# Kernel optimization log

Hardware: AMD Instinct MI355X
Metric: run time of the kernel (lower is better)

The kernel has to match this reference:

```python
import jax, jax.numpy as jnp
import numpy as np

N, E, M, NC, G = 20000, 640000, 200000, 50000, 512
VOCAB, IN, HID, OUT, NCLS = 8, 64, 128, 128, 2
EPS = 1e-5
SLOPE = 0.01


def _bn(x, g, b):
    # BatchNorm1d in training mode: biased batch statistics (matches torch normalization)
    m = jnp.mean(x, axis=0)
    v = jnp.var(x, axis=0)
    return g * (x - m) * jax.lax.rsqrt(v + EPS) + b


def _seg_softmax(a, ids, ns):
    m = jax.ops.segment_max(a, ids, num_segments=ns)
    ex = jnp.exp(a - m[ids])
    s = jax.ops.segment_sum(ex, ids, num_segments=ns)
    return ex / s[ids]


def _seg_mean(x, ids, ns):
    s = jax.ops.segment_sum(x, ids, num_segments=ns)
    c = jax.ops.segment_sum(jnp.ones((x.shape[0], 1), x.dtype), ids, num_segments=ns)
    return s / jnp.maximum(c, 1.0)


def setup_inputs() -> dict:
    key = jax.random.key(0)
    ks = jax.random.split(key, 24)

    def nrm(k, shape, fan_in):
        return jax.random.normal(k, shape, jnp.float32) * np.float32(1.0 / np.sqrt(fan_in))

    inp = {
        "sub_x": jax.random.randint(ks[0], (N, 1), 0, VOCAB),
        "sub_edge_index": jax.random.randint(ks[1], (2, E), 0, N),
        "batch": jnp.sort(jax.random.randint(ks[2], (N,), 0, G)),
        "cycle_seg_id": jnp.sort(jax.random.randint(ks[3], (M,), 0, NC)),
        "cycle_edge_idx": jax.random.randint(ks[4], (M,), 0, E),
        # embedding + mlp_feature (nn.Linear with bias)
        "emb": nrm(ks[5], (VOCAB, IN), 1),
        "w1": nrm(ks[6], (2 * IN, 2 * IN), 2 * IN), "b1": jnp.zeros((2 * IN,), jnp.float32),
        "w2": nrm(ks[7], (2 * IN, HID), 2 * IN), "b2": jnp.zeros((HID,), jnp.float32),
        "g0": jnp.ones((HID,), jnp.float32), "beta0": jnp.zeros((HID,), jnp.float32),
        # bond_agg_layer (bias-free linears)
        "watt_b": nrm(ks[8], (HID,), HID),
        "wb1": nrm(ks[9], (HID, OUT), HID), "wb2": nrm(ks[10], (OUT, OUT), OUT),
        "g1": jnp.ones((OUT,), jnp.float32), "beta1": jnp.zeros((OUT,), jnp.float32),
        # cycle_agg_layer
        "watt_c": nrm(ks[11], (HID,), HID),
        "wc1": nrm(ks[12], (HID, OUT), HID), "wc2": nrm(ks[13], (OUT, OUT), OUT),
        "g2": jnp.ones((OUT,), jnp.float32), "beta2": jnp.zeros((OUT,), jnp.float32),
        # edge_agg_layer
        "we1": nrm(ks[14], (HID, OUT), HID), "we2": nrm(ks[15], (OUT, OUT), OUT),
        "wl1": nrm(ks[16], (OUT, OUT), OUT), "wl2": nrm(ks[17], (OUT, OUT), OUT),
        "g3": jnp.ones((OUT,), jnp.float32), "beta3": jnp.zeros((OUT,), jnp.float32),
        # graph_agg_layer
        "wg1": nrm(ks[18], (OUT, OUT), OUT), "wg2": nrm(ks[19], (OUT, OUT), OUT),
        "g4": jnp.ones((OUT,), jnp.float32), "beta4": jnp.zeros((OUT,), jnp.float32),
        "wout": nrm(ks[20], (OUT, NCLS), OUT),
    }
    return inp


def reference(sub_x, sub_edge_index, batch, cycle_seg_id, cycle_edge_idx,
              emb, w1, b1, w2, b2, g0, beta0,
              watt_b, wb1, wb2, g1, beta1,
              watt_c, wc1, wc2, g2, beta2,
              we1, we2, wl1, wl2, g3, beta3,
              wg1, wg2, g4, beta4, wout):
    src, dst = sub_edge_index[0], sub_edge_index[1]
    x0 = emb[sub_x[:, 0]]                                    # [N, IN]
    h = jnp.concatenate([x0[src], x0[dst]], axis=-1)         # [E, 2*IN]
    h = (h @ w1 + b1) @ w2 + b2                              # [E, HID]
    h = jax.nn.gelu(_bn(h, g0, beta0), approximate=False)
    # bond aggregation: per-target-node segment softmax attention + scatter-mean
    ab = jax.nn.leaky_relu(h @ watt_b, SLOPE)                # [E]
    ab = _seg_softmax(ab, dst, N)
    bond = _seg_mean(ab[:, None] * h, dst, N)                # [N, HID]
    bond = jax.nn.gelu(_bn((bond @ wb1) @ wb2, g1, beta1), approximate=False)
    # cycle aggregation over membership list (cycle_seg_id: cycle id, cycle_edge_idx: edge idx)
    hc = h[cycle_edge_idx]                                   # [M, HID]
    ac = jax.nn.leaky_relu(hc @ watt_c, SLOPE)               # [M]
    ac = _seg_softmax(ac, cycle_seg_id, NC)
    cyc = _seg_mean(ac[:, None] * hc, cycle_seg_id, NC)      # [NC, HID]
    cyc = jax.nn.gelu(_bn((cyc @ wc1) @ wc2, g2, beta2), approximate=False)
    # edge update
    e = (h @ we1) @ we2                                      # [E, OUT]
    xc = jax.ops.segment_sum(cyc[cycle_seg_id], cycle_edge_idx, num_segments=E)
    e = ((e + bond[src] + bond[dst] + xc) @ wl1) @ wl2
    e = jax.nn.gelu(_bn(e, g3, beta3), approximate=False)
    # graph readout: sum edges by graph of their source node
    gsum = jax.ops.segment_sum(e, batch[src], num_segments=G)  # [G, OUT]
    gsum = (gsum @ wg1) @ wg2
    gsum = jax.nn.gelu(_bn(gsum, g4, beta4), approximate=False)
    return gsum @ wout                                       # [G, NCLS]
```

## Files before the change

kernel.cpp:

```cpp
#include <hip/hip_runtime.h>
#include <hip/hip_bf16.h>

typedef __hip_bfloat16 bf16;

__device__ __forceinline__ float b2f(bf16 v){ return __bfloat162float(v); }
__device__ __forceinline__ bf16  f2b(float v){ return __float2bfloat16(v); }
__device__ __forceinline__ float erf_fast(float x){
  const float ax=fabsf(x);
  const float t=__builtin_amdgcn_rcpf(1.f+0.3275911f*ax);
  const float p=t*(0.254829592f+t*(-0.284496736f+t*(1.421413741f+t*(-1.453152027f+t*1.061405429f))));
  const float r=1.f-p*__expf(-ax*ax);
  return copysignf(r,x);
}
__device__ __forceinline__ float geluf(float x){ return 0.5f*x*(1.0f+erf_fast(x*0.70710678118654752f)); }
__device__ __forceinline__ float lreluf(float x){ return x>0.f? x : 0.01f*x; }
__device__ __forceinline__ float bflo(unsigned u){ return __builtin_bit_cast(float,(unsigned)((u&0xFFFFu)<<16)); }
__device__ __forceinline__ float bfhi(unsigned u){ return __builtin_bit_cast(float,(unsigned)(u&0xFFFF0000u)); }
__device__ __forceinline__ unsigned packbf(float a, float b){
  bf16 ha=f2b(a), hb=f2b(b);
  return (unsigned)__builtin_bit_cast(unsigned short,ha) | ((unsigned)__builtin_bit_cast(unsigned short,hb)<<16);
}

__device__ __forceinline__ int detect_bf16(const unsigned int* words){
  int hits=0;
  for(int i=0;i<64;i++){
    unsigned u=words[i], lo=u&0xFFFFu, e=(lo>>7)&0xFFu;
    if(lo==0u || (e>=100u && e<=140u)) hits++;
  }
  return (hits>=40)?1:0;
}

struct ConvertArgs { const void* src[28]; float* dst[28]; int n[28]; };
__global__ __launch_bounds__(256) void k_convert(ConvertArgs A, const unsigned int* embw,
                                                 int* flag, float* zp, int zn){
  const int id=blockIdx.x;
  if(id<28){
    const int bf=detect_bf16(embw);
    if(id==0 && threadIdx.x==0) *flag=bf;
    const void* s=A.src[id];
    float* d=A.dst[id];
    const int n=A.n[id];
    if(bf){
      const bf16* sp=(const bf16*)s;
      for(int i=threadIdx.x;i<n;i+=256) d[i]=b2f(sp[i]);
    } else {
      const float* sp=(const float*)s;
      for(int i=threadIdx.x;i<n;i+=256) d[i]=sp[i];
    }
  } else {
    const int zb=id-28;
    int i=zb*256+threadIdx.x;
    const int stride=1024*256;
    for(;i<zn;i+=stride) zp[i]=0.f;
  }
}

struct GemmTasks5 { const float* X[5]; const float* W[5]; float* Y[5]; };

template<int K>
__global__ __launch_bounds__(256) void k_rowgemm(GemmTasks5 T5, int rows, int mode, int xPacked,
    const float* stS, const float* stQ, float invRows,
    const float* gam, const float* bet,
    float* outS, float* outQ, unsigned* Yp, const float* partsIn)
{
  constexpr int KH = K/2;
  const int task = blockIdx.y;
  const float* Xv = T5.X[task];
  const float* W  = T5.W[task];
  float* Y = T5.Y[task];
  const int tid = threadIdx.x, c = tid & 127, kh = tid >> 7;
  __shared__ float redSQ[256];
  if(mode==1 && partsIn){
    float s=0.f;
    for(int k=0;k<64;k++) s+=partsIn[k*256+tid];
    redSQ[tid]=s;
    __syncthreads();
  }
  float wreg[KH];
  #pragma unroll
  for(int i=0;i<KH;i++) wreg[i]=W[(kh*KH+i)*128+c];
  __shared__ float xls[8*K];
  __shared__ float part[2*8*128];
  float ls=0.f, lq=0.f;
  const int nbatch=(rows+7)>>3;
  for (int b=blockIdx.x; b<nbatch; b+=gridDim.x){
    const int base=b*8;
    for (int idx=tid; idx<8*K; idx+=256){
      const int row=idx/K, k=idx-row*K, r=base+row;
      float v=0.f;
      if (r<rows){
        if(xPacked){
          const unsigned u=((const unsigned*)Xv)[(size_t)r*(K/2)+(k>>1)];
          v = (k&1) ? bfhi(u) : bflo(u);
        } else {
          v = Xv[(size_t)r*K+k];
        }
        if (mode==1){
          const float sv = partsIn ? redSQ[k]     : stS[k];
          const float qv = partsIn ? redSQ[128+k] : stQ[k];
          float mn=sv*invRows;
          float vr=fmaxf(qv*invRows-mn*mn,0.f);
          float sc=gam[k]*rsqrtf(vr+1e-5f);
          float sh=bet[k]-mn*sc;
          v=geluf(v*sc+sh);
        }
      }
      xls[idx]=v;
    }
    __syncthreads();
    #pragma unroll
    for (int rr=0;rr<8;rr++){
      const float* xp=&xls[rr*K+kh*KH];
      float acc=0.f;
      #pragma unroll
      for (int j=0;j<KH;j+=4){
        const float4 xv=*(const float4*)(xp+j);
        acc += wreg[j]*xv.x + wreg[j+1]*xv.y + wreg[j+2]*xv.z + wreg[j+3]*xv.w;
      }
      part[kh*1024 + rr*128 + c]=acc;
    }
    __syncthreads();
    if (Yp==nullptr){
      #pragma unroll
      for (int q=0;q<4;q++){
        const int r=kh*4+q, row=base+r;
        if (row<rows){
          float y=part[r*128+c]+part[1024+r*128+c];
          Y[row*128+c]=y;
          ls+=y; lq+=y*y;
        }
      }
      __syncthreads();
    } else {
      if constexpr (K==128){
        #pragma unroll
        for (int q=0;q<4;q++){
          const int r=kh*4+q, row=base+r;
          float y=0.f;
          if (row<rows){
            y=part[r*128+c]+part[1024+r*128+c];
            ls+=y; lq+=y*y;
          }
          xls[r*128+c]=y;
        }
        __syncthreads();
        for (int idx=tid; idx<512; idx+=256){
          const int r2=idx>>6, j=idx&63, row=base+r2;
          if(row<rows) Yp[(size_t)row*64+j]=packbf(xls[r2*128+2*j],xls[r2*128+2*j+1]);
        }
        __syncthreads();
      }
    }
  }
  if (outS){ atomicAdd(&outS[c],ls); atomicAdd(&outQ[c],lq); }
}

struct RGDual {
  const float* x0; int rows0; int pk0; float inv0; const float* g0; const float* b0;
  unsigned* yp0; const float* parts0;
  const float* x1; int rows1; int pk1; float inv1; const float* g1; const float* b1;
  unsigned* yp1; const float* parts1;
  const float* W;
};
__global__ __launch_bounds__(512) void k_rowgemm_dual(RGDual D)
{
  const int tid = threadIdx.x, c = tid & 127, kq = tid >> 7;
  __shared__ float scs0[128], shs0[128], scs1[128], shs1[128];
  if(tid<256){
    const int t=tid>>7, k=tid&127;
    const float* partsIn = t ? D.parts1 : D.parts0;
    float s=0.f,q=0.f;
    for(int j=0;j<64;j++){ s+=partsIn[j*256+k]; }
    for(int j=0;j<64;j++){ q+=partsIn[j*256+128+k]; }
    const float invRows = t ? D.inv1 : D.inv0;
    const float gam = (t ? D.g1 : D.g0)[k];
    const float bet = (t ? D.b1 : D.b0)[k];
    const float mn=s*invRows;
    const float vr=fmaxf(q*invRows-mn*mn,0.f);
    const float sc=gam*rsqrtf(vr+1e-5f);
    const float sh=bet-mn*sc;
    if(t){ scs1[k]=sc; shs1[k]=sh; } else { scs0[k]=sc; shs0[k]=sh; }
  }
  __syncthreads();
  float wreg[32];
  #pragma unroll
  for(int i=0;i<32;i++) wreg[i]=D.W[(kq*32+i)*128+c];
  __shared__ float xls[8*128];
  __shared__ float part[4*8*128];
  const int TB0=(D.rows0+7)>>3, TB1=(D.rows1+7)>>3;
  const int TBT=TB0+TB1;
  for (int gb=blockIdx.x; gb<TBT; gb+=gridDim.x){
    const int t1=(gb>=TB0);
    const int b = t1 ? gb-TB0 : gb;
    const float* Xv = t1 ? D.x1 : D.x0;
    const int rows  = t1 ? D.rows1 : D.rows0;
    const int xPacked = t1 ? D.pk1 : D.pk0;
    unsigned* Yp = t1 ? D.yp1 : D.yp0;
    const float* scs = t1 ? scs1 : scs0;
    const float* shs = t1 ? shs1 : shs0;
    const int base=b*8;
    for (int idx=tid; idx<8*128; idx+=512){
      const int row=idx>>7, k=idx&127, r=base+row;
      float v=0.f;
      if (r<rows){
        if(xPacked){
          const unsigned u=((const unsigned*)Xv)[(size_t)r*64+(k>>1)];
          v = (k&1) ? bfhi(u) : bflo(u);
        } else {
          v = Xv[(size_t)r*128+k];
        }
        v=geluf(v*scs[k]+shs[k]);
      }
      xls[idx]=v;
    }
    __syncthreads();
    float acc[8];
    #pragma unroll
    for (int rr=0;rr<8;rr++){
      const float* xp=&xls[rr*128+kq*32];
      float a=0.f;
      #pragma unroll
      for (int j=0;j<32;j+=4){
        const float4 xv=*(const float4*)(xp+j);
        a += wreg[j]*xv.x + wreg[j+1]*xv.y + wreg[j+2]*xv.z + wreg[j+3]*xv.w;
      }
      acc[rr]=a;
    }
    #pragma unroll
    for (int rr=0;rr<8;rr++) part[kq*1024+rr*128+c]=acc[rr];
    __syncthreads();
    #pragma unroll
    for (int q=0;q<2;q++){
      const int r=kq*2+q, row=base+r;
      const float y=(part[r*128+c]+part[1024+r*128+c])
                   +(part[2048+r*128+c]+part[3072+r*128+c]);
      const float y2=__shfl_xor(y,1,64);
      if(((tid&1)==0) && row<rows) Yp[(size_t)row*64+(c>>1)]=packbf(y,y2);
    }
  }
}

__global__ __launch_bounds__(256) void k_table_T(const float* emb, const float* w1, const float* b1,
                                                 const float* w2, const float* b2, float* T)
{
  __shared__ float A[2048];
  const int tid=threadIdx.x;
  for (int idx=tid; idx<2048; idx+=256){
    const int half=idx>>10, rem=idx&1023, s=rem>>7, j=rem&127;
    float acc=0.f;
    for(int k=0;k<64;k++) acc += emb[s*64+k]*w1[(half*64+k)*128+j];
    A[idx]=acc;
  }
  __syncthreads();
  const int o=tid&127;
  for(int rr=tid>>7; rr<8; rr+=2){
    const int r=blockIdx.x*8+rr, s=r>>3, d=r&7;
    float acc=b2[o];
    for(int j=0;j<128;j++){
      float t1=A[s*128+j]+A[1024+d*128+j]+b1[j];
      acc+=t1*w2[j*128+o];
    }
    T[r*128+o]=acc;
  }
}

#define SCH 1024

__global__ __launch_bounds__(256) void k_edge_code(const int* sx, const int* src, const int* dst,
    const int* batch, unsigned char* code, unsigned short* gg, int* cnt64, int* ns,
    int* blockHist, int E)
{
  __shared__ int hist[64];
  __shared__ int gh[512];
  const int tid=threadIdx.x;
  if(tid<64) hist[tid]=0;
  for(int i=tid;i<512;i+=256) gh[i]=0;
  __syncthreads();
  const int base=blockIdx.x*SCH;
  #pragma unroll
  for(int u=0;u<SCH/256;u++){
    const int e=base+u*256+tid;
    if(e<E){
      const int s_=src[e], d_=dst[e];
      const int sc=sx[s_], dc=sx[d_];
      const int cd=sc*8+dc;
      code[e]=(unsigned char)cd;
      const int gb=batch[s_];
      gg[e]=(unsigned short)gb;
      atomicAdd(&hist[cd],1);
      atomicAdd(&ns[d_*8+sc],1);
      atomicAdd(&gh[gb],1);
    }
  }
  __syncthreads();
  if(tid<64){ int h=hist[tid]; if(h) atomicAdd(&cnt64[tid],h); }
  for(int i=tid;i<512;i+=256) blockHist[blockIdx.x*512+i]=gh[i];
}

__global__ __launch_bounds__(256) void k_gscan_col(int* blockHist, int* gtot, int NB){
  const int g=blockIdx.x;
  const int tid=threadIdx.x;
  __shared__ int sd[256];
  int run=0;
  for(int base=0;base<NB;base+=256){
    const int b=base+tid;
    const int v=(b<NB)?blockHist[(size_t)b*512+g]:0;
    sd[tid]=v; __syncthreads();
    for(int d=1;d<256;d<<=1){ int t=(tid>=d)?sd[tid-d]:0; __syncthreads(); sd[tid]+=t; __syncthreads(); }
    const int incl=sd[tid];
    const int tot=sd[255];
    if(b<NB) blockHist[(size_t)b*512+g]=run+incl-v;
    __syncthreads();
    run+=tot;
  }
  if(tid==0) gtot[g]=run;
}

__global__ __launch_bounds__(256) void k_gscatter(const unsigned short* gg, const int* blockHist,
    const int* gtot, const unsigned char* code, const int* src, const int* dst,
    unsigned short* sortedG, int* posE, unsigned long long* recP, int E){
  __shared__ int baseg[512];
  __shared__ int sg[512];
  const int tid=threadIdx.x;
  for(int i=tid;i<512;i+=256) sg[i]=gtot[i];
  __syncthreads();
  for(int d=1;d<512;d<<=1){
    int t0[2];
    for(int i=tid,j=0;i<512;i+=256,j++) t0[j]=(i>=d)?sg[i-d]:0;
    __syncthreads();
    for(int i=tid,j=0;i<512;i+=256,j++) sg[i]+=t0[j];
    __syncthreads();
  }
  for(int i=tid;i<512;i+=256) baseg[i]=blockHist[blockIdx.x*512+i]+sg[i]-gtot[i];
  __syncthreads();
  const int base=blockIdx.x*SCH;
  for(int i=tid;i<SCH;i+=256){
    const int e=base+i;
    if(e<E){
      const int g=gg[e];
      const int p=atomicAdd(&baseg[g],1);
      sortedG[p]=(unsigned short)g;
      posE[e]=p;
      recP[p]=(unsigned long long)code[e] | ((unsigned long long)(unsigned)src[e]<<8)
            | ((unsigned long long)(unsigned)dst[e]<<32);
    }
  }
}

__global__ __launch_bounds__(256) void k_htable(const float* T, const int* cnt64,
    const float* g0, const float* beta0, const float* wattb, const float* wattc,
    float* h_table, float* abt, float* act, float* ea, int E)
{
  __shared__ float h[64*132];
  __shared__ float cw[64];
  const int tid=threadIdx.x;
  if(tid<64) cw[tid]=(float)cnt64[tid];
  __syncthreads();
  const int c=tid&127;
  const float invE=1.f/(float)E;
  float s=0.f,q=0.f;
  for(int r2=0;r2<64;r2++){ float v=T[r2*128+c]; float w=cw[r2]; s+=w*v; q+=w*v*v; }
  const float mn=s*invE, vr=fmaxf(q*invE-mn*mn,0.f);
  const float sc=g0[c]*rsqrtf(vr+1e-5f), sh=beta0[c]-mn*sc;
  for(int r=tid>>7; r<64; r+=2){
    float v=geluf(T[r*128+c]*sc+sh);
    h[r*132+c]=v;
    h_table[r*128+c]=v;
  }
  __syncthreads();
  if(tid<64){
    float sb=0.f,scc=0.f;
    for(int k=0;k<128;k++){ float hv=h[tid*132+k]; sb+=hv*wattb[k]; scc+=hv*wattc[k]; }
    const float ab_=lreluf(sb), ac_=lreluf(scc);
    abt[tid]=ab_; act[tid]=ac_;
    float mx=ac_;
    #pragma unroll
    for(int o=1;o<64;o<<=1) mx=fmaxf(mx,__shfl_xor(mx,o,64));
    ea[tid]=expf(ac_-mx);
  }
}

__global__ __launch_bounds__(256) void k_cycle_hist(const int* cseg, const int* cidx,
    const unsigned char* code, const int* posE, int* nsc, int* cntP, int M)
{
  const int base=blockIdx.x*1024+threadIdx.x;
  #pragma unroll
  for(int u=0;u<4;u++){
    const int m=base+u*256;
    if(m<M){
      const int e=cidx[m];
      atomicAdd(&nsc[cseg[m]*64 + (int)code[e]],1);
      atomicAdd(&cntP[posE[e]],1);
    }
  }
}

__global__ __launch_bounds__(256) void k_bond(const int* ns, const int* sx, const float* abt,
    const float* hWb, float* bm, float* parts, int N)
{
  const int tid=threadIdx.x, c=tid&127, grp=tid>>7;
  float ls=0.f,lq=0.f;
  const int base=blockIdx.x*16+grp*8;
  for(int i=0;i<8;i++){
    const int n=base+i;
    if(n>=N) break;
    const int d=sx[n];
    float cnt=0.f, mx=-1e30f, nsv[8];
    #pragma unroll
    for(int s=0;s<8;s++){ float v=(float)ns[n*8+s]; nsv[s]=v; cnt+=v; if(v>0.f) mx=fmaxf(mx,abt[s*8+d]); }
    float y=0.f;
    if(cnt>0.f){
      float ssum=0.f, ex[8];
      #pragma unroll
      for(int s=0;s<8;s++){ ex[s]= nsv[s]>0.f ? nsv[s]*expf(abt[s*8+d]-mx) : 0.f; ssum+=ex[s]; }
      const float inv=1.f/(ssum*cnt);
      #pragma unroll
      for(int s=0;s<8;s++){ if(ex[s]>0.f) y += (ex[s]*inv)*hWb[(s*8+d)*128+c]; }
    }
    bm[n*128+c]=y;
    ls+=y; lq+=y*y;
  }
  __shared__ float sS[128], sQ[128];
  if(tid<128){ sS[tid]=0.f; sQ[tid]=0.f; }
  __syncthreads();
  atomicAdd(&sS[c],ls); atomicAdd(&sQ[c],lq);
  __syncthreads();
  if(tid<128){
    float* slot=&parts[(size_t)(blockIdx.x&63)*256];
    atomicAdd(&slot[tid],sS[tid]); atomicAdd(&slot[128+tid],sQ[tid]);
  }
}

__global__ __launch_bounds__(256) void k_cyc(const int* nsc, const float* ea,
    const float* hWc, unsigned* ucm, float* parts, int NC)
{
  const int tid=threadIdx.x, c=tid&127, kh=tid>>7;
  const int lane=tid&63;
  const int wv4=tid>>6;
  const float eaL=ea[lane];
  float wreg[32];
  #pragma unroll
  for(int i=0;i<32;i++) wreg[i]=hWc[(kh*32+i)*128+c]*ea[kh*32+i];
  __shared__ float cnts[512];
  __shared__ float part[2*8*128];
  __shared__ float invcs[8];
  float ls=0.f,lq=0.f;
  const int nbatch=(NC+7)>>3;
  for(int b=blockIdx.x;b<nbatch;b+=gridDim.x){
    const int base=b*8;
    for(int i=tid;i<512;i+=256){
      const int seg=base+(i>>6);
      cnts[i] = (seg<NC) ? (float)nsc[(size_t)seg*64+(i&63)] : 0.f;
    }
    __syncthreads();
    #pragma unroll
    for(int rr2=0;rr2<2;rr2++){
      const int r=wv4*2+rr2;
      const float n=cnts[r*64+lane];
      float S=n*eaL, C=n;
      #pragma unroll
      for(int o=1;o<64;o<<=1){ S+=__shfl_xor(S,o,64); C+=__shfl_xor(C,o,64); }
      if(lane==0) invcs[r]=(C>0.f&&S>0.f)?1.f/(S*C):0.f;
    }
    #pragma unroll
    for(int rr=0;rr<8;rr++){
      const float* xp=&cnts[rr*64+kh*32];
      float acc=0.f;
      #pragma unroll
      for(int j=0;j<32;j+=4){
        const float4 xv=*(const float4*)(xp+j);
        acc += wreg[j]*xv.x + wreg[j+1]*xv.y + wreg[j+2]*xv.z + wreg[j+3]*xv.w;
      }
      part[kh*1024+rr*128+c]=acc;
    }
    __syncthreads();
    #pragma unroll
    for(int q=0;q<4;q++){
      const int r=kh*4+q, row=base+r;
      float y=0.f;
      if(row<NC){
        y=(part[r*128+c]+part[1024+r*128+c])*invcs[r];
        ls+=y; lq+=y*y;
      }
      const float y2=__shfl_xor(y,1,64);
      if(((lane&1)==0) && row<NC) ucm[(size_t)row*64+(c>>1)]=packbf(y,y2);
    }
    __syncthreads();
  }
  __shared__ float sS[128], sQ[128];
  if(tid<128){ sS[tid]=0.f; sQ[tid]=0.f; }
  __syncthreads();
  atomicAdd(&sS[c],ls); atomicAdd(&sQ[c],lq);
  __syncthreads();
  if(tid<128){
    float* slot=&parts[(size_t)(blockIdx.x&63)*256];
    atomicAdd(&slot[tid],sS[tid]); atomicAdd(&slot[128+tid],sQ[tid]);
  }
}

__global__ __launch_bounds__(256) void k_scan_block(const int* cntP, int* blkSum, int E){
  __shared__ int sd[256];
  const int tid=threadIdx.x, base=blockIdx.x*1024;
  int s=0;
  for(int q=0;q<4;q++){ int i=base+tid*4+q; if(i<E) s+=cntP[i]; }
  sd[tid]=s; __syncthreads();
  for(int d=1;d<256;d<<=1){ int t=(tid>=d)?sd[tid-d]:0; __syncthreads(); sd[tid]+=t; __syncthreads(); }
  if(tid==255) blkSum[blockIdx.x]=sd[255];
}

__global__ __launch_bounds__(256) void k_scan_mid(const int* blkSum, int* blkOff, int nb){
  __shared__ int sd[1024];
  const int tid=threadIdx.x;
  for(int i=tid;i<1024;i+=256) sd[i]=(i<nb)?blkSum[i]:0;
  __syncthreads();
  for(int d=1;d<1024;d<<=1){
    int t[4];
    for(int i=tid,j=0;i<1024;i+=256,j++) t[j]=(i>=d)?sd[i-d]:0;
    __syncthreads();
    for(int i=tid,j=0;i<1024;i+=256,j++) sd[i]+=t[j];
    __syncthreads();
  }
  for(int i=tid;i<nb;i+=256) blkOff[i]=sd[i]-blkSum[i];
}

__global__ __launch_bounds__(256) void k_scan_write(const int* cntP, const int* blkOff,
                                                    int* offP, int E, int M){
  __shared__ int sd[256];
  const int tid=threadIdx.x, base=blockIdx.x*1024;
  int v[4]; int s=0;
  for(int q=0;q<4;q++){ int i=base+tid*4+q; v[q]=(i<E)?cntP[i]:0; s+=v[q]; }
  sd[tid]=s; __syncthreads();
  for(int d=1;d<256;d<<=1){ int t=(tid>=d)?sd[tid-d]:0; __syncthreads(); sd[tid]+=t; __syncthreads(); }
  int run=blkOff[blockIdx.x]+sd[tid]-s;
  for(int q=0;q<4;q++){ int i=base+tid*4+q; if(i<E) offP[i]=run; run+=v[q]; }
  if(blockIdx.x==0&&tid==0) offP[E]=M;
}

__global__ __launch_bounds__(256) void k_place(const int* cseg, const int* cidx, const int* posE,
                                               const int* offP, int* cursor, int* entrySeg, int M){
  const int base=blockIdx.x*1024+threadIdx.x;
  #pragma unroll
  for(int u=0;u<4;u++){
    const int m=base+u*256;
    if(m<M){
      const int p=posE[cidx[m]];
      const int pos=offP[p]+atomicAdd(&cursor[p],1);
      entrySeg[pos]=cseg[m];
    }
  }
}

__global__ __launch_bounds__(256) void k_pass1_store(const unsigned long long* recP,
    const float* eLt, const unsigned* ubond, const unsigned* ucyc,
    const int* offP, const int* entrySeg, unsigned* vbuf, float* parts,
    int E, int upx)
{
  const int tid=threadIdx.x;
  const int lane=tid&63, wave=tid>>6;
  const int xcd=blockIdx.x&7;
  const int wix=(blockIdx.x>>3)*4+wave;
  const int NU=(E+15)>>4;
  int u0=xcd*upx + (int)(((long long)wix*(long long)upx)>>10);
  int u1=xcd*upx + (int)(((long long)(wix+1)*(long long)upx)>>10);
  if(u0>NU)u0=NU; if(u1>NU)u1=NU;
  int e=u0*16; const int e1=(u1*16<E)?u1*16:E;
  float lsx=0.f,lsy=0.f,lqx=0.f,lqy=0.f;
  while(e<e1){
    int nv=e1-e; if(nv>64)nv=64;
    const int t=e+((lane<nv)?lane:(nv-1));
    const unsigned long long r0=recP[t];
    const unsigned rlo=(unsigned)r0, rhi=(unsigned)(r0>>32);
    const int oa0=offP[t], ob0=offP[t+1];
    int i=0;
    for(; i+8<=nv; i+=8){
      unsigned lo[8],hi[8]; int a[8],b[8];
      #pragma unroll
      for(int q=0;q<8;q++){
        lo[q]=(unsigned)__builtin_amdgcn_readlane((int)rlo,i+q);
        hi[q]=(unsigned)__builtin_amdgcn_readlane((int)rhi,i+q);
        a[q]=__builtin_amdgcn_readlane(oa0,i+q);
        b[q]=__builtin_amdgcn_readlane(ob0,i+q);
      }
      float2 ea[8]; unsigned ub[8],ud[8];
      #pragma unroll
      for(int q=0;q<8;q++){
        ea[q]=((const float2*)(eLt+(size_t)(lo[q]&0xFFu)*128))[lane];
        ub[q]=ubond[(size_t)(lo[q]>>8)*64+lane];
        ud[q]=ubond[(size_t)hi[q]*64+lane];
      }
      #pragma unroll
      for(int q=0;q<8;q++){
        float x=ea[q].x+bflo(ub[q])+bflo(ud[q]);
        float y=ea[q].y+bfhi(ub[q])+bfhi(ud[q]);
        for(int j=a[q];j<b[q];j++){
          const unsigned w=ucyc[(size_t)entrySeg[j]*64+lane];
          x+=bflo(w); y+=bfhi(w);
        }
        lsx+=x; lqx+=x*x; lsy+=y; lqy+=y*y;
        vbuf[(size_t)(e+i+q)*64+lane]=packbf(x,y);
      }
    }
    for(; i<nv; i++){
      const unsigned lo=(unsigned)__builtin_amdgcn_readlane((int)rlo,i);
      const unsigned hi=(unsigned)__builtin_amdgcn_readlane((int)rhi,i);
      const int a=__builtin_amdgcn_readlane(oa0,i);
      const int b=__builtin_amdgcn_readlane(ob0,i);
      const float2 ea2=((const float2*)(eLt+(size_t)(lo&0xFFu)*128))[lane];
      const unsigned ub=ubond[(size_t)(lo>>8)*64+lane];
      const unsigned ud=ubond[(size_t)hi*64+lane];
      float x=ea2.x+bflo(ub)+bflo(ud);
      float y=ea2.y+bfhi(ub)+bfhi(ud);
      for(int j=a;j<b;j++){
        const unsigned w=ucyc[(size_t)entrySeg[j]*64+lane];
        x+=bflo(w); y+=bfhi(w);
      }
      lsx+=x; lqx+=x*x; lsy+=y; lqy+=y*y;
      vbuf[(size_t)(e+i)*64+lane]=packbf(x,y);
    }
    e+=nv;
  }
  __shared__ float sS[128], sQ[128];
  if(tid<128){ sS[tid]=0.f; sQ[tid]=0.f; }
  __syncthreads();
  const int c0=lane*2;
  atomicAdd(&sS[c0],lsx); atomicAdd(&sS[c0+1],lsy);
  atomicAdd(&sQ[c0],lqx); atomicAdd(&sQ[c0+1],lqy);
  __syncthreads();
  if(tid<128){
    float* slot=&parts[(size_t)(blockIdx.x&63)*256];
    atomicAdd(&slot[tid],sS[tid]); atomicAdd(&slot[128+tid],sQ[tid]);
  }
}

__global__ __launch_bounds__(256) void k_pass2_stream(const uint2* vbuf2,
    const unsigned short* sortedG, const float* parts,
    const float* g3, const float* beta3, float* gsum, int E)
{
  __shared__ float sSQ[256];
  const int tid=threadIdx.x;
  {
    float s=0.f;
    #pragma unroll 8
    for(int k=0;k<64;k++) s+=parts[k*256+tid];
    sSQ[tid]=s;
  }
  __syncthreads();
  const int lane=tid&63, wave=tid>>6;
  const int half=lane>>5;
  const int l32=lane&31;
  const int cb=l32*4;
  const float invE=1.f/(float)E;
  float sc[4],sh[4];
  #pragma unroll
  for(int k2=0;k2<4;k2++){
    const int c=cb+k2;
    float mn=sSQ[c]*invE, vr=fmaxf(sSQ[128+c]*invE-mn*mn,0.f);
    sc[k2]=g3[c]*rsqrtf(vr+1e-5f); sh[k2]=beta3[c]-mn*sc[k2];
  }
  const int wix=blockIdx.x*4+wave;
  const int NP=(E+1)>>1;
  int i0=(int)(((long long)wix*(long long)NP)>>13)*2;
  int i1=(int)(((long long)(wix+1)*(long long)NP)>>13)*2;
  if(i1>E)i1=E;
  int gcur=-1; float a0=0.f,a1=0.f,a2=0.f,a3=0.f;
  int i=i0;
  for(; i+32<=i1; i+=32){
    int gq[16]; uint2 uq[16];
    #pragma unroll
    for(int q=0;q<16;q++) gq[q]=sortedG[i+2*q+half];
    #pragma unroll
    for(int q=0;q<16;q++) uq[q]=vbuf2[(size_t)(i+2*q+half)*32+l32];
    #pragma unroll
    for(int q=0;q<16;q++){
      if(gq[q]!=gcur){
        if(gcur>=0){
          atomicAdd(&gsum[gcur*128+cb+0],a0); atomicAdd(&gsum[gcur*128+cb+1],a1);
          atomicAdd(&gsum[gcur*128+cb+2],a2); atomicAdd(&gsum[gcur*128+cb+3],a3);
        }
        gcur=gq[q]; a0=a1=a2=a3=0.f;
      }
      a0+=geluf(fmaf(bflo(uq[q].x),sc[0],sh[0]));
      a1+=geluf(fmaf(bfhi(uq[q].x),sc[1],sh[1]));
      a2+=geluf(fmaf(bflo(uq[q].y),sc[2],sh[2]));
      a3+=geluf(fmaf(bfhi(uq[q].y),sc[3],sh[3]));
    }
  }
  for(; i<i1; i+=2){
    const int p=i+half;
    if(p>=E) break;
    const int g=sortedG[p];
    const uint2 u=vbuf2[(size_t)p*32+l32];
    if(g!=gcur){
      if(gcur>=0){
        atomicAdd(&gsum[gcur*128+cb+0],a0); atomicAdd(&gsum[gcur*128+cb+1],a1);
        atomicAdd(&gsum[gcur*128+cb+2],a2); atomicAdd(&gsum[gcur*128+cb+3],a3);
      }
      gcur=g; a0=a1=a2=a3=0.f;
    }
    a0+=geluf(fmaf(bflo(u.x),sc[0],sh[0])); a1+=geluf(fmaf(bfhi(u.x),sc[1],sh[1]));
    a2+=geluf(fmaf(bflo(u.y),sc[2],sh[2])); a3+=geluf(fmaf(bfhi(u.y),sc[3],sh[3]));
  }
  if(gcur>=0){
    atomicAdd(&gsum[gcur*128+cb+0],a0); atomicAdd(&gsum[gcur*128+cb+1],a1);
    atomicAdd(&gsum[gcur*128+cb+2],a2); atomicAdd(&gsum[gcur*128+cb+3],a3);
  }
}

__global__ __launch_bounds__(256) void k_out(const float* gw, const float* st4S, const float* st4Q,
    const float* g4, const float* beta4, const float* wout, void* out, const int* flag, int G)
{
  const int lane=threadIdx.x&63;
  const int r=blockIdx.x*4 + (threadIdx.x>>6);
  const float invG=1.f/(float)G;
  float a0=0.f,a1=0.f;
  #pragma unroll
  for(int h=0;h<2;h++){
    const int k=lane+64*h;
    const float mn=st4S[k]*invG;
    const float vr=fmaxf(st4Q[k]*invG-mn*mn,0.f);
    const float sc=g4[k]*rsqrtf(vr+1e-5f), sh=beta4[k]-mn*sc;
    const float v=geluf(gw[r*128+k]*sc+sh);
    a0+=v*wout[k*2+0]; a1+=v*wout[k*2+1];
  }
  for(int o=1;o<64;o<<=1){ a0+=__shfl_xor(a0,o,64); a1+=__shfl_xor(a1,o,64); }
  if(lane==0){
    if(*flag){ ((bf16*)out)[r*2+0]=f2b(a0); ((bf16*)out)[r*2+1]=f2b(a1); }
    else     { ((float*)out)[r*2+0]=a0;     ((float*)out)[r*2+1]=a1; }
  }
}

extern "C" void kernel_launch(void* const* d_in, const int* in_sizes, int n_in,
                              void* d_out, int out_size, void* d_ws, size_t ws_size,
                              hipStream_t stream)
{
  const int N  = in_sizes[0];
  const int E  = in_sizes[1]/2;
  const int M  = in_sizes[3];
  const int NC = 50000;
  const int G  = 512;

  const int* sub_x=(const int*)d_in[0];
  const int* src=(const int*)d_in[1];
  const int* dst=src+E;
  const int* batch=(const int*)d_in[2];
  const int* cseg=(const int*)d_in[3];
  const int* cidx=(const int*)d_in[4];

  char* ws=(char*)d_ws;
  size_t off=0;
  auto carve=[&](size_t bytes)->char*{ char* p=ws+off; off=(off+bytes+255)&~(size_t)255; return p; };

  size_t ftot=0;
  for(int i=0;i<28;i++) ftot += (size_t)in_sizes[5+i];
  float* stage=(float*)carve(ftot*4);
  float* fin[28];
  { size_t so=0; for(int i=0;i<28;i++){ fin[i]=stage+so; so+=(size_t)in_sizes[5+i]; } }
  const float *emb_f=fin[0], *w1_f=fin[1], *b1_f=fin[2], *w2_f=fin[3], *b2_f=fin[4],
              *g0_f=fin[5], *beta0_f=fin[6], *wattb_f=fin[7], *wb1_f=fin[8], *wb2_f=fin[9],
              *g1_f=fin[10], *beta1_f=fin[11], *wattc_f=fin[12], *wc1_f=fin[13], *wc2_f=fin[14],
              *g2_f=fin[15], *beta2_f=fin[16], *we1_f=fin[17], *we2_f=fin[18], *wl1_f=fin[19],
              *wl2_f=fin[20], *g3_f=fin[21], *beta3_f=fin[22], *wg1_f=fin[23], *wg2_f=fin[24],
              *g4_f=fin[25], *beta4_f=fin[26], *wout_f=fin[27];

  int* flag=(int*)carve(256);
  float* Wb =(float*)carve(65536);
  float* Wc =(float*)carve(65536);
  float* Wl =(float*)carve(65536);
  float* Wg =(float*)carve(65536);
  float* We =(float*)carve(65536);
  float* Wel=(float*)carve(65536);
  float* T      =(float*)carve(64*128*4);
  float* h_table=(float*)carve(64*128*4);
  float* hWb    =(float*)carve(64*128*4);
  float* hWc    =(float*)carve(64*128*4);
  float* eLt    =(float*)carve(64*128*4);
  float* abt=(float*)carve(256);
  float* act=(float*)carve(256);
  float* eaT=(float*)carve(256);
  float* bm   =(float*)carve((size_t)N*128*4);
  unsigned* ucm=(unsigned*)carve((size_t)NC*64*4);
  unsigned* ubond=(unsigned*)carve((size_t)N*64*4);
  unsigned* ucyc =(unsigned*)carve((size_t)NC*64*4);
  unsigned char* code=(unsigned char*)carve((size_t)E);
  unsigned short* gg=(unsigned short*)carve((size_t)E*2);
  unsigned short* sortedG=(unsigned short*)carve((size_t)E*2);
  int*   posE  =(int*)carve((size_t)E*4);
  unsigned long long* recP=(unsigned long long*)carve((size_t)E*8);
  int*   offP  =(int*)carve((size_t)(E+1)*4);
  int*   entrySeg=(int*)carve((size_t)M*4);
  int*   blkSum=(int*)carve(4096);
  int*   blkOff=(int*)carve(4096);
  int*   gtot  =(int*)carve(2048);
  const int NB=(E+SCH-1)/SCH;
  int*   blockHist=(int*)carve((size_t)NB*512*4);
  float* gw  =(float*)carve((size_t)G*128*4);

  const size_t zStart=off;
  int*   cnt64=(int*)carve(256);
  float* stats=(float*)carve(4096);
  float* st4S=stats+6*128, *st4Q=stats+7*128;
  float* parts1=(float*)carve(64*256*4);
  float* parts2=(float*)carve(64*256*4);
  float* parts3=(float*)carve(64*256*4);
  float* gsum=(float*)carve((size_t)G*128*4);
  int*   ns   =(int*)carve((size_t)N*8*4);
  int*   nsc  =(int*)carve((size_t)NC*64*4);
  int*   cntP =(int*)carve((size_t)E*4);
  int*   cursor=(int*)carve((size_t)E*4);
  const size_t zEnd=off;

  unsigned* vbuf=(unsigned*)carve((size_t)E*64*4);
  const int haveV = (off <= ws_size) ? 1 : 0;
  (void)n_in; (void)out_size;

  {
    ConvertArgs A{};
    for(int i=0;i<28;i++){ A.src[i]=d_in[5+i]; A.dst[i]=fin[i]; A.n[i]=in_sizes[5+i]; }
    k_convert<<<28+1024,256,0,stream>>>(A,(const unsigned int*)d_in[5],flag,
                                        (float*)(ws+zStart),(int)((zEnd-zStart)/4));
  }

  k_table_T<<<8,256,0,stream>>>(emb_f,w1_f,b1_f,w2_f,b2_f,T);

  {
    GemmTasks5 t{};
    t.X[0]=wb1_f; t.W[0]=wb2_f; t.Y[0]=Wb;
    t.X[1]=wc1_f; t.W[1]=wc2_f; t.Y[1]=Wc;
    t.X[2]=wl1_f; t.W[2]=wl2_f; t.Y[2]=Wl;
    t.X[3]=wg1_f; t.W[3]=wg2_f; t.Y[3]=Wg;
    t.X[4]=we1_f; t.W[4]=we2_f; t.Y[4]=We;
    k_rowgemm<128><<<dim3(16,5),256,0,stream>>>(t,128,0,0,nullptr,nullptr,0.f,nullptr,nullptr,nullptr,nullptr,nullptr,nullptr);
  }
  {
    GemmTasks5 t{};
    t.X[0]=We; t.W[0]=Wl; t.Y[0]=Wel;
    k_rowgemm<128><<<dim3(16,1),256,0,stream>>>(t,128,0,0,nullptr,nullptr,0.f,nullptr,nullptr,nullptr,nullptr,nullptr,nullptr);
  }

  k_edge_code<<<NB,256,0,stream>>>(sub_x,src,dst,batch,code,gg,cnt64,ns,blockHist,E);
  k_gscan_col<<<512,256,0,stream>>>(blockHist,gtot,NB);
  k_gscatter<<<NB,256,0,stream>>>(gg,blockHist,gtot,code,src,dst,sortedG,posE,recP,E);
  k_htable<<<1,256,0,stream>>>(T,cnt64,g0_f,beta0_f,wattb_f,wattc_f,h_table,abt,act,eaT,E);
  {
    GemmTasks5 t{};
    t.X[0]=h_table; t.W[0]=Wb;  t.Y[0]=hWb;
    t.X[1]=h_table; t.W[1]=Wc;  t.Y[1]=hWc;
    t.X[2]=h_table; t.W[2]=Wel; t.Y[2]=eLt;
    k_rowgemm<128><<<dim3(8,3),256,0,stream>>>(t,64,0,0,nullptr,nullptr,0.f,nullptr,nullptr,nullptr,nullptr,nullptr,nullptr);
  }
  k_cycle_hist<<<(M+1023)/1024,256,0,stream>>>(cseg,cidx,code,posE,nsc,cntP,M);
  k_bond<<<(N+15)/16,256,0,stream>>>(ns,sub_x,abt,hWb,bm,parts1,N);
  k_cyc<<<2048,256,0,stream>>>(nsc,eaT,hWc,ucm,parts2,NC);
  {
    RGDual D{};
    D.x0=bm;                 D.rows0=N;  D.pk0=0; D.inv0=1.f/(float)N;  D.g0=g1_f; D.b0=beta1_f; D.yp0=ubond; D.parts0=parts1;
    D.x1=(const float*)ucm;  D.rows1=NC; D.pk1=1; D.inv1=1.f/(float)NC; D.g1=g2_f; D.b1=beta2_f; D.yp1=ucyc;  D.parts1=parts2;
    D.W=Wl;
    k_rowgemm_dual<<<2048,512,0,stream>>>(D);
  }
  const int nb=(E+1023)/1024;
  k_scan_block<<<nb,256,0,stream>>>(cntP,blkSum,E);
  k_scan_mid<<<1,256,0,stream>>>(blkSum,blkOff,nb);
  k_scan_write<<<nb,256,0,stream>>>(cntP,blkOff,offP,E,M);
  k_place<<<(M+1023)/1024,256,0,stream>>>(cseg,cidx,posE,offP,cursor,entrySeg,M);
  {
    const int NU=(E+15)/16;
    const int upx=(NU+7)/8;
    k_pass1_store<<<2048,256,0,stream>>>(recP,eLt,ubond,ucyc,offP,entrySeg,
                                         haveV?vbuf:(unsigned*)cursor,parts3,E,upx);
    k_pass2_stream<<<2048,256,0,stream>>>((const uint2*)vbuf,sortedG,parts3,
                                          g3_f,beta3_f,gsum,E);
  }
  {
    GemmTasks5 t{};
    t.X[0]=gsum; t.W[0]=Wg; t.Y[0]=gw;
    k_rowgemm<128><<<dim3(64,1),256,0,stream>>>(t,G,0,0,nullptr,nullptr,0.f,nullptr,nullptr,st4S,st4Q,nullptr,nullptr);
  }
  k_out<<<G/4,256,0,stream>>>(gw,st4S,st4Q,g4_f,beta4_f,wout_f,d_out,flag,G);
}
```

Before: 583.7 us.

## Use bf16 MFMA in dual row GEMM for bond and cycle transforms

Rewrites k_rowgemm_dual so it uses MFMA 16x16x32 bf16 instructions instead of scalar FP32 FMAs with a four-way K split and an LDS reduction. Each block now covers 16 rows with 256 threads. Weights are held in registers as bf16 fragments, and GELU-normalized inputs are staged in LDS as bf16. This cuts the ALU work and removes the partial-sum shared-memory reduction, at the cost of bf16 rounding on the weights and inputs to this GEMM. It is one kernel inside a larger pipeline, so its effect on total time may be small.

```diff
diff --git a/kernel.cpp b/kernel.cpp
--- a/kernel.cpp
+++ b/kernel.cpp
@@ -2,6 +2,8 @@
 #include <hip/hip_bf16.h>
 
 typedef __hip_bfloat16 bf16;
+typedef __attribute__((ext_vector_type(4))) float f32x4;
+typedef __attribute__((ext_vector_type(8))) short bf16x8;
 
 __device__ __forceinline__ float b2f(bf16 v){ return __bfloat162float(v); }
 __device__ __forceinline__ bf16  f2b(float v){ return __float2bfloat16(v); }
@@ -162,11 +164,13 @@
   unsigned* yp1; const float* parts1;
   const float* W;
 };
-__global__ __launch_bounds__(512) void k_rowgemm_dual(RGDual D)
-{
-  const int tid = threadIdx.x, c = tid & 127, kq = tid >> 7;
+__global__ __launch_bounds__(256) void k_rowgemm_dual(RGDual D)
+{
+  const int tid=threadIdx.x;
+  const int lane=tid&63, wave=tid>>6;
+  const int l15=lane&15, lhi=lane>>4;
   __shared__ float scs0[128], shs0[128], scs1[128], shs1[128];
-  if(tid<256){
+  {
     const int t=tid>>7, k=tid&127;
     const float* partsIn = t ? D.parts1 : D.parts0;
     float s=0.f,q=0.f;
@@ -181,13 +185,22 @@
     const float sh=bet-mn*sc;
     if(t){ scs1[k]=sc; shs1[k]=sh; } else { scs0[k]=sc; shs0[k]=sh; }
   }
-  __syncthreads();
-  float wreg[32];
+  bf16x8 breg[2][4];
   #pragma unroll
-  for(int i=0;i<32;i++) wreg[i]=D.W[(kq*32+i)*128+c];
-  __shared__ float xls[8*128];
-  __shared__ float part[4*8*128];
-  const int TB0=(D.rows0+7)>>3, TB1=(D.rows1+7)>>3;
+  for(int ct=0;ct<2;ct++){
+    const int col=(wave*2+ct)*16 + l15;
+    #pragma unroll
+    for(int ks=0;ks<4;ks++){
+      const int kb=ks*32 + lhi*8;
+      #pragma unroll
+      for(int i=0;i<8;i++){
+        breg[ct][ks][i]=__builtin_bit_cast(short, f2b(D.W[(size_t)(kb+i)*128+col]));
+      }
+    }
+  }
+  __syncthreads();
+  __shared__ short xtile[16*136];
+  const int TB0=(D.rows0+15)>>4, TB1=(D.rows1+15)>>4;
   const int TBT=TB0+TB1;
   for (int gb=blockIdx.x; gb<TBT; gb+=gridDim.x){
     const int t1=(gb>=TB0);
@@ -198,45 +211,44 @@
     unsigned* Yp = t1 ? D.yp1 : D.yp0;
     const float* scs = t1 ? scs1 : scs0;
     const float* shs = t1 ? shs1 : shs0;
-    const int base=b*8;
-    for (int idx=tid; idx<8*128; idx+=512){
-      const int row=idx>>7, k=idx&127, r=base+row;
-      float v=0.f;
+    const int base=b*16;
+    for (int idx=tid; idx<1024; idx+=256){
+      const int row=idx>>6, kp=idx&63, k0=kp*2, r=base+row;
+      float v0=0.f,v1=0.f;
       if (r<rows){
         if(xPacked){
-          const unsigned u=((const unsigned*)Xv)[(size_t)r*64+(k>>1)];
-          v = (k&1) ? bfhi(u) : bflo(u);
+          const unsigned u=((const unsigned*)Xv)[(size_t)r*64+kp];
+          v0=bflo(u); v1=bfhi(u);
         } else {
-          v = Xv[(size_t)r*128+k];
+          const float2 xv=((const float2*)(Xv+(size_t)r*128))[kp];
+          v0=xv.x; v1=xv.y;
         }
-        v=geluf(v*scs[k]+shs[k]);
-      }
-      xls[idx]=v;
-    }
-    __syncthreads();
-    float acc[8];
-    #pragma unroll
-    for (int rr=0;rr<8;rr++){
-      const float* xp=&xls[rr*128+kq*32];
-      float a=0.f;
-      #pragma unroll
-      for (int j=0;j<32;j+=4){
-        const float4 xv=*(const float4*)(xp+j);
-        a += wreg[j]*xv.x + wreg[j+1]*xv.y + wreg[j+2]*xv.z + wreg[j+3]*xv.w;
-      }
-      acc[rr]=a;
-    }
-    #pragma unroll
-    for (int rr=0;rr<8;rr++) part[kq*1024+rr*128+c]=acc[rr];
-    __syncthreads();
-    #pragma unroll
-    for (int q=0;q<2;q++){
-      const int r=kq*2+q, row=base+r;
-      const float y=(part[r*128+c]+part[1024+r*128+c])
-                   +(part[2048+r*128+c]+part[3072+r*128+c]);
-      const float y2=__shfl_xor(y,1,64);
-      if(((tid&1)==0) && row<rows) Yp[(size_t)row*64+(c>>1)]=packbf(y,y2);
-    }
+        v0=geluf(v0*scs[k0]+shs[k0]);
+        v1=geluf(v1*scs[k0+1]+shs[k0+1]);
+      }
+      ((unsigned*)xtile)[row*68+kp]=packbf(v0,v1);
+    }
+    __syncthreads();
+    f32x4 acc0={0.f,0.f,0.f,0.f}, acc1={0.f,0.f,0.f,0.f};
+    #pragma unroll
+    for(int ks=0;ks<4;ks++){
+      const bf16x8 afrag = *reinterpret_cast<const bf16x8*>(&xtile[l15*136 + ks*32 + lhi*8]);
+      acc0=__builtin_amdgcn_mfma_f32_16x16x32_bf16(afrag,breg[0][ks],acc0,0,0,0);
+      acc1=__builtin_amdgcn_mfma_f32_16x16x32_bf16(afrag,breg[1][ks],acc1,0,0,0);
+    }
+    #pragma unroll
+    for(int j=0;j<4;j++){
+      const int row=base+lhi*4+j;
+      const float ya=acc0[j];
+      const float ya2=__shfl_xor(ya,1,64);
+      if(((lane&1)==0) && row<rows)
+        Yp[(size_t)row*64 + (wave*2+0)*8 + (l15>>1)]=packbf(ya,ya2);
+      const float yb=acc1[j];
+      const float yb2=__shfl_xor(yb,1,64);
+      if(((lane&1)==0) && row<rows)
+        Yp[(size_t)row*64 + (wave*2+1)*8 + (l15>>1)]=packbf(yb,yb2);
+    }
+    __syncthreads();
   }
 }
 
@@ -856,7 +868,7 @@
     D.x0=bm;                 D.rows0=N;  D.pk0=0; D.inv0=1.f/(float)N;  D.g0=g1_f; D.b0=beta1_f; D.yp0=ubond; D.parts0=parts1;
     D.x1=(const float*)ucm;  D.rows1=NC; D.pk1=1; D.inv1=1.f/(float)NC; D.g1=g2_f; D.b1=beta2_f; D.yp1=ucyc;  D.parts1=parts2;
     D.W=Wl;
-    k_rowgemm_dual<<<2048,512,0,stream>>>(D);
+    k_rowgemm_dual<<<2048,256,0,stream>>>(D);
   }
   const int nb=(E+1023)/1024;
   k_scan_block<<<nb,256,0,stream>>>(cntP,blkSum,E);
```

New measurement: 559.5 us. 4.2% less time.
